# Performance work log

Hardware: AMD Instinct MI355X
Metric: run time of the kernel (lower is better)

Reference implementation:

```python
import jax, jax.numpy as jnp
import numpy as np

B, N = 128, 64
HID, MLP, DS, DV = 128, 128, 32, 32
DH = MLP - DS - DV  # 64
FILL = -10.0


def _embed_mask(x, W, b, fill):
    # Linear+ReLU on non-NaN rows; fill NaN rows with `fill` (matches embed_with_masking).
    nan = jnp.isnan(x).any(-1)
    e = jax.nn.relu(jnp.where(jnp.isnan(x), 0.0, x) @ W + b)
    return jnp.where(nan[..., None], jnp.asarray(fill, x.dtype), e)


def setup_inputs() -> dict:
    key = jax.random.key(0)
    ks = jax.random.split(key, 12)
    s = 0.05
    return {
        "hidden_states": jax.random.normal(ks[0], (B, N, HID), jnp.float32),
        "obs1": jax.random.normal(ks[1], (B, N, 2), jnp.float32),
        "obs2": jax.random.normal(ks[2], (B, N, 2), jnp.float32),
        "w_sp": jax.random.normal(ks[3], (2, DS), jnp.float32) * s,
        "b_sp": jnp.zeros((DS,), jnp.float32),
        "w_vel": jax.random.normal(ks[4], (2, DV), jnp.float32) * s,
        "b_vel": jnp.zeros((DV,), jnp.float32),
        "w_hid": jax.random.normal(ks[5], (HID, DH), jnp.float32) * s,
        "b_hid": jnp.zeros((DH,), jnp.float32),
        "wq": jax.random.normal(ks[6], (MLP, MLP), jnp.float32) * s,
        "wk": jax.random.normal(ks[7], (MLP, MLP), jnp.float32) * s,
        "wv": jax.random.normal(ks[8], (MLP, MLP), jnp.float32) * s,
        "in_proj_w": jax.random.normal(ks[9], (MLP, 3 * MLP), jnp.float32) * s,
        "in_proj_b": jnp.zeros((3 * MLP,), jnp.float32),
        "mha_out_w": jax.random.normal(ks[10], (MLP, MLP), jnp.float32) * s,
        "mha_out_b": jnp.zeros((MLP,), jnp.float32),
        "out_w": jax.random.normal(ks[11], (MLP, MLP), jnp.float32) * s,
        "out_b": jnp.zeros((MLP,), jnp.float32),
    }


def reference(hidden_states, obs1, obs2, w_sp, b_sp, w_vel, b_vel, w_hid, b_hid,
              wq, wk, wv, in_proj_w, in_proj_b, mha_out_w, mha_out_b, out_w, out_b):
    b, n = obs2.shape[0], obs2.shape[1]
    # relative positions: rel[b,i,j] = obs2[b,j] - obs2[b,i]
    rel = obs2[:, None, :, :] - obs2[:, :, None, :]              # [B,N,N,2]
    sp = _embed_mask(rel, w_sp, b_sp, FILL)                      # [B,N,N,DS]
    hid = _embed_mask(hidden_states, w_hid, b_hid, 0.0)          # [B,N,DH]
    hid_unf = jnp.broadcast_to(hid[:, None, :, :], (b, n, n, DH))
    vel = obs2 - obs1
    relvel = vel[:, None, :, :] - vel[:, :, None, :]             # [B,N,N,2]
    dv = _embed_mask(relvel * 4, w_vel, b_vel, FILL)             # [B,N,N,DV]
    emb = jnp.concatenate([sp, hid_unf, dv], axis=-1)            # [B,N,N,MLP]

    # MHA (1 head) in-proj weights split (stored as [in,out])
    w_iq, w_ik, w_iv = in_proj_w[:, :MLP], in_proj_w[:, MLP:2 * MLP], in_proj_w[:, 2 * MLP:]
    b_iq, b_ik, b_iv = in_proj_b[:MLP], in_proj_b[MLP:2 * MLP], in_proj_b[2 * MLP:]

    # Only the diagonal query position is kept by the final eye-mask gather,
    # and softmax rows are independent, so compute q only at j == i.
    idx = jnp.arange(n)
    emb_diag = emb[:, idx, idx]                                  # [B,N,MLP]
    q = (emb_diag @ wq) @ w_iq + b_iq                            # [B,N,MLP]
    k = (emb @ wk) @ w_ik + b_ik                                 # [B,N,N,MLP]
    v = (emb @ wv) @ w_iv + b_iv                                 # [B,N,N,MLP]

    scores = jnp.einsum('bid,bijd->bij', q, k) / jnp.sqrt(jnp.asarray(MLP, q.dtype))
    attn = jax.nn.softmax(scores, axis=-1)                       # [B,N,N]
    ctx = jnp.einsum('bij,bijd->bid', attn, v)                   # [B,N,MLP]
    mha_out = ctx @ mha_out_w + mha_out_b
    out = mha_out @ out_w + out_b                                # [B,N,out_dim]
    return out.reshape(b * n, -1)
```

## Files before the change

### kernel.cpp

```cpp
#include <hip/hip_runtime.h>

#define WS_WQC   0
#define WS_WKC   16384
#define WS_WVC   32768
#define WS_MOW   49152
#define WS_GQ    65536
#define WS_G0Q   73728
#define WS_FALL  73856
#define WS_FB    90240
#define WS_HID   90368
#define WS_NEED_HID_BYTES ((size_t)(90368 + 128*64*64) * 4)

__global__ __launch_bounds__(256) void precompute1(
    const float* __restrict__ wq, const float* __restrict__ wk,
    const float* __restrict__ wv, const float* __restrict__ in_proj_w,
    const float* __restrict__ mha_out_w, const float* __restrict__ out_w,
    const float* __restrict__ hs, const float* __restrict__ w_hid,
    const float* __restrict__ b_hid, float* __restrict__ ws)
{
    __shared__ __align__(16) float sbuf[4224];
    const int tid = threadIdx.x;

    if (blockIdx.x < 256) {
        const int mat  = blockIdx.x >> 6;
        const int rp   = blockIdx.x & 63;
        const int rsel = tid >> 7;
        const int col  = tid & 127;
        const int r    = 2 * rp + rsel;
        const float* A; const float* Bm; int ldb; float* C;
        if (mat == 0)      { A = wq;        Bm = in_proj_w;       ldb = 384; C = ws + WS_WQC; }
        else if (mat == 1) { A = wk;        Bm = in_proj_w + 128; ldb = 384; C = ws + WS_WKC; }
        else if (mat == 2) { A = wv;        Bm = in_proj_w + 256; ldb = 384; C = ws + WS_WVC; }
        else               { A = mha_out_w; Bm = out_w;           ldb = 128; C = ws + WS_MOW; }
        sbuf[tid] = A[r * 128 + col];
        __syncthreads();
        float acc = 0.f;
        #pragma unroll 8
        for (int d = 0; d < 128; ++d) acc = fmaf(sbuf[rsel * 128 + d], Bm[d * ldb + col], acc);
        C[r * 128 + col] = acc;
    } else {
        const int b2 = blockIdx.x - 256;
        const int b = b2 >> 1, half = b2 & 1;
        const float4* src = (const float4*)(hs + b * 8192 + half * 4096);
        for (int k = tid; k < 1024; k += 256) {
            const int row = k >> 5, c = k & 31;
            *(float4*)&sbuf[row * 132 + 4 * c] = src[k];
        }
        __syncthreads();
        const int ty = tid >> 4, tx = tid & 15;
        float a0c[4] = {0,0,0,0}, a1c[4] = {0,0,0,0};
        for (int d0 = 0; d0 < 128; d0 += 4) {
            const float4 a0 = *(const float4*)&sbuf[(2*ty+0)*132 + d0];
            const float4 a1 = *(const float4*)&sbuf[(2*ty+1)*132 + d0];
            const float* a0p = (const float*)&a0;
            const float* a1p = (const float*)&a1;
            #pragma unroll
            for (int dd = 0; dd < 4; ++dd) {
                const float4 w4 = *(const float4*)&w_hid[(d0+dd)*64 + 4*tx];
                a0c[0] = fmaf(a0p[dd], w4.x, a0c[0]); a0c[1] = fmaf(a0p[dd], w4.y, a0c[1]);
                a0c[2] = fmaf(a0p[dd], w4.z, a0c[2]); a0c[3] = fmaf(a0p[dd], w4.w, a0c[3]);
                a1c[0] = fmaf(a1p[dd], w4.x, a1c[0]); a1c[1] = fmaf(a1p[dd], w4.y, a1c[1]);
                a1c[2] = fmaf(a1p[dd], w4.z, a1c[2]); a1c[3] = fmaf(a1p[dd], w4.w, a1c[3]);
            }
        }
        const float4 bh = *(const float4*)&b_hid[4*tx];
        float* dst = ws + WS_HID + b * 4096 + (32*half + 2*ty) * 64 + 4*tx;
        *(float4*)dst        = make_float4(fmaxf(a0c[0]+bh.x,0.f), fmaxf(a0c[1]+bh.y,0.f),
                                           fmaxf(a0c[2]+bh.z,0.f), fmaxf(a0c[3]+bh.w,0.f));
        *(float4*)(dst + 64) = make_float4(fmaxf(a1c[0]+bh.x,0.f), fmaxf(a1c[1]+bh.y,0.f),
                                           fmaxf(a1c[2]+bh.z,0.f), fmaxf(a1c[3]+bh.w,0.f));
    }
}

__global__ __launch_bounds__(128) void precompute2(
    const float* __restrict__ b_sp, const float* __restrict__ b_vel,
    const float* __restrict__ in_proj_b, const float* __restrict__ mha_out_b,
    const float* __restrict__ out_w, const float* __restrict__ out_b,
    float* __restrict__ ws)
{
    const float* Wqc = ws + WS_WQC;
    const float* Wkc = ws + WS_WKC;
    const float* Wvc = ws + WS_WVC;
    const float* Mow = ws + WS_MOW;
    const int bid = blockIdx.x, tid = threadIdx.x;
    __shared__ float sa[128];

    if (bid < 64) {
        const int k = bid;
        sa[tid] = Wqc[(32 + k) * 128 + tid];
        __syncthreads();
        const int j = tid;
        const int pj = (j < 64) ? 32 + j : ((j < 96) ? j - 64 : j);
        const float* brow = Wkc + pj * 128;
        float acc = 0.f;
        #pragma unroll 8
        for (int d = 0; d < 128; ++d) acc = fmaf(sa[d], brow[d], acc);
        ws[WS_GQ + k * 128 + j] = acc;
    } else if (bid < 192) {
        const int k2 = bid - 64;
        const int srcRow = (k2 < 32) ? k2 : ((k2 < 64) ? 96 + (k2 - 32) : 32 + (k2 - 64));
        sa[tid] = Wvc[srcRow * 128 + tid];
        __syncthreads();
        float acc = 0.f;
        #pragma unroll 8
        for (int m = 0; m < 128; ++m) acc = fmaf(sa[m], Mow[m * 128 + tid], acc);
        ws[WS_FALL + k2 * 128 + tid] = acc;
    } else if (bid == 192) {
        float acc = out_b[tid];
        #pragma unroll 8
        for (int m = 0; m < 128; ++m) {
            acc = fmaf(in_proj_b[256 + m], Mow[m * 128 + tid], acc);
            acc = fmaf(mha_out_b[m], out_w[m * 128 + tid], acc);
        }
        ws[WS_FB + tid] = acc;
    } else {
        float qc = in_proj_b[tid];
        #pragma unroll 4
        for (int s = 0; s < 32; ++s) {
            qc = fmaf(fmaxf(b_sp[s], 0.f),  Wqc[s * 128 + tid], qc);
            qc = fmaf(fmaxf(b_vel[s], 0.f), Wqc[(96 + s) * 128 + tid], qc);
        }
        sa[tid] = qc;
        __syncthreads();
        const int j = tid;
        const int pj = (j < 64) ? 32 + j : ((j < 96) ? j - 64 : j);
        const float* brow = Wkc + pj * 128;
        float acc = 0.f;
        #pragma unroll 8
        for (int d = 0; d < 128; ++d) acc = fmaf(sa[d], brow[d], acc);
        ws[WS_G0Q + j] = acc;
    }
}

#define L_OBS  4224
#define L_WV   4480

template <bool HIDWS>
__global__ __launch_bounds__(256) void attn_main(
    const float* __restrict__ hs, const float* __restrict__ obs1,
    const float* __restrict__ obs2,
    const float* __restrict__ w_sp, const float* __restrict__ b_sp,
    const float* __restrict__ w_vel, const float* __restrict__ b_vel,
    const float* __restrict__ w_hid, const float* __restrict__ b_hid,
    const float* __restrict__ ws, float* __restrict__ out)
{
    const int tid = threadIdx.x;
    const int l   = tid & 63;
    const int w   = tid >> 6;
    const int b   = blockIdx.x >> 3;
    const int i0  = (blockIdx.x & 7) * 8;

    const float* GQ   = ws + WS_GQ;
    const float* g0q  = ws + WS_G0Q;
    const float* Fall = ws + WS_FALL;
    const float* fbv  = ws + WS_FB;

    __shared__ __align__(16) float smem[6016];
    float* const s_hid = smem;
    float* const s_obs = smem + L_OBS;
    float* const tt = smem + L_WV + w * 384;
    float* const qq = smem + L_WV + w * 384 + 128;
    float* const aa = smem + L_WV + w * 384 + 256;

    if (tid < 64) {
        const int g = b * 64 + tid;
        const float2 o2 = ((const float2*)obs2)[g];
        const float2 o1 = ((const float2*)obs1)[g];
        *(float4*)&s_obs[tid * 4] = make_float4(o2.x, o2.y, o2.x - o1.x, o2.y - o1.y);
    }
    if (HIDWS) {
        const float4* src = (const float4*)(ws + WS_HID + b * 4096);
        #pragma unroll
        for (int k = tid; k < 1024; k += 256) {
            const int row = k >> 4, c4 = (k & 15) * 4;
            const float4 v = src[k];
            *(float2*)&s_hid[row * 66 + c4]     = make_float2(v.x, v.y);
            *(float2*)&s_hid[row * 66 + c4 + 2] = make_float2(v.z, v.w);
        }
    } else {
        const int r = tid >> 2, qseg = (tid & 3) * 16;
        float acc[16];
        #pragma unroll
        for (int c = 0; c < 16; ++c) acc[c] = b_hid[qseg + c];
        for (int k = 0; k < 128; ++k) {
            const float a = hs[b * 8192 + r * 128 + k];
            #pragma unroll
            for (int c4 = 0; c4 < 4; ++c4) {
                const float4 w4 = *(const float4*)&w_hid[k * 64 + qseg + 4 * c4];
                acc[4*c4+0] = fmaf(a, w4.x, acc[4*c4+0]);
                acc[4*c4+1] = fmaf(a, w4.y, acc[4*c4+1]);
                acc[4*c4+2] = fmaf(a, w4.z, acc[4*c4+2]);
                acc[4*c4+3] = fmaf(a, w4.w, acc[4*c4+3]);
            }
        }
        #pragma unroll
        for (int c = 0; c < 16; c += 2)
            *(float2*)&s_hid[r * 66 + qseg + c] =
                make_float2(fmaxf(acc[c], 0.f), fmaxf(acc[c+1], 0.f));
    }
    __syncthreads();

    const int rg0 = i0 + 2 * w;

    {
        const float2 bias = *(const float2*)&g0q[2 * l];
        float a00 = bias.x, a01 = bias.y, a10 = bias.x, a11 = bias.y;
        const float* h0p = &s_hid[rg0 * 66];
        const float* h1p = &s_hid[(rg0 + 1) * 66];
        for (int k0 = 0; k0 < 64; k0 += 2) {
            const float2 h0 = *(const float2*)&h0p[k0];
            const float2 h1 = *(const float2*)&h1p[k0];
            const float2 g0v = *(const float2*)&GQ[k0 * 128 + 2 * l];
            const float2 g1v = *(const float2*)&GQ[(k0 + 1) * 128 + 2 * l];
            a00 = fmaf(h0.x, g0v.x, fmaf(h0.y, g1v.x, a00));
            a01 = fmaf(h0.x, g0v.y, fmaf(h0.y, g1v.y, a01));
            a10 = fmaf(h1.x, g0v.x, fmaf(h1.y, g1v.x, a10));
            a11 = fmaf(h1.x, g0v.y, fmaf(h1.y, g1v.y, a11));
        }
        if (l < 32) {
            *(float2*)&tt[2 * l]      = make_float2(a00, a01);
            *(float2*)&tt[64 + 2 * l] = make_float2(a10, a11);
        } else {
            *(float2*)&qq[2 * l - 64]  = make_float2(a00, a01);
            *(float2*)&qq[2 * l]       = make_float2(a10, a11);
        }
    }

    float sc0 = 0.f, sc1 = 0.f;
    {
        const float* hlp = &s_hid[l * 66];
        for (int c0 = 0; c0 < 64; c0 += 4) {
            const float4 t0 = *(const float4*)&tt[c0];
            const float4 t1 = *(const float4*)&tt[64 + c0];
            const float2 ha = *(const float2*)&hlp[c0];
            const float2 hb = *(const float2*)&hlp[c0 + 2];
            sc0 = fmaf(t0.x, ha.x, fmaf(t0.y, ha.y, fmaf(t0.z, hb.x, fmaf(t0.w, hb.y, sc0))));
            sc1 = fmaf(t1.x, ha.x, fmaf(t1.y, ha.y, fmaf(t1.z, hb.x, fmaf(t1.w, hb.y, sc1))));
        }
    }

    {
        const float4 oj  = *(const float4*)&s_obs[4 * l];
        const float4 oiA = *(const float4*)&s_obs[4 * rg0];
        const float4 oiB = *(const float4*)&s_obs[4 * (rg0 + 1)];
        const float rxA = oj.x - oiA.x, ryA = oj.y - oiA.y;
        const float dxA = (oj.z - oiA.z) * 4.f, dyA = (oj.w - oiA.w) * 4.f;
        const float rxB = oj.x - oiB.x, ryB = oj.y - oiB.y;
        const float dxB = (oj.z - oiB.z) * 4.f, dyB = (oj.w - oiB.w) * 4.f;
        float e0 = 0.f, e1 = 0.f;
        for (int s0 = 0; s0 < 32; s0 += 4) {
            const float4 qsA = *(const float4*)&qq[s0];
            const float4 qsB = *(const float4*)&qq[64 + s0];
            const float4 qdA = *(const float4*)&qq[32 + s0];
            const float4 qdB = *(const float4*)&qq[96 + s0];
            const float4 w0  = *(const float4*)&w_sp[s0];
            const float4 w1  = *(const float4*)&w_sp[32 + s0];
            const float4 bs  = *(const float4*)&b_sp[s0];
            const float4 wv0 = *(const float4*)&w_vel[s0];
            const float4 wv1 = *(const float4*)&w_vel[32 + s0];
            const float4 bv  = *(const float4*)&b_vel[s0];
            e0 = fmaf(qsA.x, fmaxf(fmaf(rxA, w0.x, fmaf(ryA, w1.x, bs.x)), 0.f), e0);
            e0 = fmaf(qsA.y, fmaxf(fmaf(rxA, w0.y, fmaf(ryA, w1.y, bs.y)), 0.f), e0);
            e0 = fmaf(qsA.z, fmaxf(fmaf(rxA, w0.z, fmaf(ryA, w1.z, bs.z)), 0.f), e0);
            e0 = fmaf(qsA.w, fmaxf(fmaf(rxA, w0.w, fmaf(ryA, w1.w, bs.w)), 0.f), e0);
            e0 = fmaf(qdA.x, fmaxf(fmaf(dxA, wv0.x, fmaf(dyA, wv1.x, bv.x)), 0.f), e0);
            e0 = fmaf(qdA.y, fmaxf(fmaf(dxA, wv0.y, fmaf(dyA, wv1.y, bv.y)), 0.f), e0);
            e0 = fmaf(qdA.z, fmaxf(fmaf(dxA, wv0.z, fmaf(dyA, wv1.z, bv.z)), 0.f), e0);
            e0 = fmaf(qdA.w, fmaxf(fmaf(dxA, wv0.w, fmaf(dyA, wv1.w, bv.w)), 0.f), e0);
            e1 = fmaf(qsB.x, fmaxf(fmaf(rxB, w0.x, fmaf(ryB, w1.x, bs.x)), 0.f), e1);
            e1 = fmaf(qsB.y, fmaxf(fmaf(rxB, w0.y, fmaf(ryB, w1.y, bs.y)), 0.f), e1);
            e1 = fmaf(qsB.z, fmaxf(fmaf(rxB, w0.z, fmaf(ryB, w1.z, bs.z)), 0.f), e1);
            e1 = fmaf(qsB.w, fmaxf(fmaf(rxB, w0.w, fmaf(ryB, w1.w, bs.w)), 0.f), e1);
            e1 = fmaf(qdB.x, fmaxf(fmaf(dxB, wv0.x, fmaf(dyB, wv1.x, bv.x)), 0.f), e1);
            e1 = fmaf(qdB.y, fmaxf(fmaf(dxB, wv0.y, fmaf(dyB, wv1.y, bv.y)), 0.f), e1);
            e1 = fmaf(qdB.z, fmaxf(fmaf(dxB, wv0.z, fmaf(dyB, wv1.z, bv.z)), 0.f), e1);
            e1 = fmaf(qdB.w, fmaxf(fmaf(dxB, wv0.w, fmaf(dyB, wv1.w, bv.w)), 0.f), e1);
        }
        const float scale = 0.08838834764831845f;
        float v0 = (sc0 + e0) * scale;
        float v1 = (sc1 + e1) * scale;
        float m0 = v0, m1 = v1;
        #pragma unroll
        for (int off = 32; off > 0; off >>= 1) {
            m0 = fmaxf(m0, __shfl_xor(m0, off, 64));
            m1 = fmaxf(m1, __shfl_xor(m1, off, 64));
        }
        const float ex0 = __expf(v0 - m0);
        const float ex1 = __expf(v1 - m1);
        float su0 = ex0, su1 = ex1;
        #pragma unroll
        for (int off = 32; off > 0; off >>= 1) {
            su0 += __shfl_xor(su0, off, 64);
            su1 += __shfl_xor(su1, off, 64);
        }
        *(float2*)&aa[2 * l] = make_float2(ex0 / su0, ex1 / su1);
    }

    {
        const int r = l >> 5, s = l & 31;
        const float w0 = w_sp[s],       w1 = w_sp[32 + s],  bsv = b_sp[s];
        const float u0 = w_vel[s],      u1 = w_vel[32 + s], bvv = b_vel[s];
        const float4 oi = *(const float4*)&s_obs[4 * (rg0 + r)];
        float ssp = 0.f, sdv = 0.f;
        for (int j0 = 0; j0 < 64; j0 += 2) {
            const float4 av  = *(const float4*)&aa[2 * j0];
            const float4 oj0 = *(const float4*)&s_obs[4 * j0];
            const float4 oj1 = *(const float4*)&s_obs[4 * j0 + 4];
            const float a0 = r ? av.y : av.x;
            const float a1 = r ? av.w : av.z;
            {
                const float rx = oj0.x - oi.x, ry = oj0.y - oi.y;
                const float dx = (oj0.z - oi.z) * 4.f, dy = (oj0.w - oi.w) * 4.f;
                ssp = fmaf(a0, fmaxf(fmaf(rx, w0, fmaf(ry, w1, bsv)), 0.f), ssp);
                sdv = fmaf(a0, fmaxf(fmaf(dx, u0, fmaf(dy, u1, bvv)), 0.f), sdv);
            }
            {
                const float rx = oj1.x - oi.x, ry = oj1.y - oi.y;
                const float dx = (oj1.z - oi.z) * 4.f, dy = (oj1.w - oi.w) * 4.f;
                ssp = fmaf(a1, fmaxf(fmaf(rx, w0, fmaf(ry, w1, bsv)), 0.f), ssp);
                sdv = fmaf(a1, fmaxf(fmaf(dx, u0, fmaf(dy, u1, bvv)), 0.f), sdv);
            }
        }
        tt[r * 64 + s]      = ssp;
        tt[r * 64 + 32 + s] = sdv;
    }

    {
        float ah0 = 0.f, ah1 = 0.f;
        for (int j0 = 0; j0 < 64; j0 += 2) {
            const float4 av = *(const float4*)&aa[2 * j0];
            const float h0 = s_hid[j0 * 66 + l];
            const float h1 = s_hid[(j0 + 1) * 66 + l];
            ah0 = fmaf(av.x, h0, fmaf(av.z, h1, ah0));
            ah1 = fmaf(av.y, h0, fmaf(av.w, h1, ah1));
        }
        qq[l]      = ah0;
        qq[64 + l] = ah1;
    }

    {
        const float2 fb2 = *(const float2*)&fbv[2 * l];
        float o00 = fb2.x, o01 = fb2.y, o10 = fb2.x, o11 = fb2.y;
        for (int k0 = 0; k0 < 64; k0 += 4) {
            const float4 A0 = *(const float4*)&tt[k0];
            const float4 A1 = *(const float4*)&tt[64 + k0];
            const float2 f0 = *(const float2*)&Fall[k0 * 128 + 2 * l];
            const float2 f1 = *(const float2*)&Fall[(k0 + 1) * 128 + 2 * l];
            const float2 f2 = *(const float2*)&Fall[(k0 + 2) * 128 + 2 * l];
            const float2 f3 = *(const float2*)&Fall[(k0 + 3) * 128 + 2 * l];
            o00 = fmaf(A0.x, f0.x, fmaf(A0.y, f1.x, fmaf(A0.z, f2.x, fmaf(A0.w, f3.x, o00))));
            o01 = fmaf(A0.x, f0.y, fmaf(A0.y, f1.y, fmaf(A0.z, f2.y, fmaf(A0.w, f3.y, o01))));
            o10 = fmaf(A1.x, f0.x, fmaf(A1.y, f1.x, fmaf(A1.z, f2.x, fmaf(A1.w, f3.x, o10))));
            o11 = fmaf(A1.x, f0.y, fmaf(A1.y, f1.y, fmaf(A1.z, f2.y, fmaf(A1.w, f3.y, o11))));
        }
        for (int k0 = 0; k0 < 64; k0 += 4) {
            const float4 A0 = *(const float4*)&qq[k0];
            const float4 A1 = *(const float4*)&qq[64 + k0];
            const float2 f0 = *(const float2*)&Fall[(64 + k0) * 128 + 2 * l];
            const float2 f1 = *(const float2*)&Fall[(65 + k0) * 128 + 2 * l];
            const float2 f2 = *(const float2*)&Fall[(66 + k0) * 128 + 2 * l];
            const float2 f3 = *(const float2*)&Fall[(67 + k0) * 128 + 2 * l];
            o00 = fmaf(A0.x, f0.x, fmaf(A0.y, f1.x, fmaf(A0.z, f2.x, fmaf(A0.w, f3.x, o00))));
            o01 = fmaf(A0.x, f0.y, fmaf(A0.y, f1.y, fmaf(A0.z, f2.y, fmaf(A0.w, f3.y, o01))));
            o10 = fmaf(A1.x, f0.x, fmaf(A1.y, f1.x, fmaf(A1.z, f2.x, fmaf(A1.w, f3.x, o10))));
            o11 = fmaf(A1.x, f0.y, fmaf(A1.y, f1.y, fmaf(A1.z, f2.y, fmaf(A1.w, f3.y, o11))));
        }
        const int gr = (b * 64 + rg0) * 128 + 2 * l;
        *(float2*)&out[gr]       = make_float2(o00, o01);
        *(float2*)&out[gr + 128] = make_float2(o10, o11);
    }
}

extern "C" void kernel_launch(void* const* d_in, const int* in_sizes, int n_in,
                              void* d_out, int out_size, void* d_ws, size_t ws_size,
                              hipStream_t stream) {
    const float* hs        = (const float*)d_in[0];
    const float* obs1      = (const float*)d_in[1];
    const float* obs2      = (const float*)d_in[2];
    const float* w_sp      = (const float*)d_in[3];
    const float* b_sp      = (const float*)d_in[4];
    const float* w_vel     = (const float*)d_in[5];
    const float* b_vel     = (const float*)d_in[6];
    const float* w_hid     = (const float*)d_in[7];
    const float* b_hid     = (const float*)d_in[8];
    const float* wq        = (const float*)d_in[9];
    const float* wk        = (const float*)d_in[10];
    const float* wv        = (const float*)d_in[11];
    const float* in_proj_w = (const float*)d_in[12];
    const float* in_proj_b = (const float*)d_in[13];
    const float* mha_out_w = (const float*)d_in[14];
    const float* mha_out_b = (const float*)d_in[15];
    const float* out_w     = (const float*)d_in[16];
    const float* out_b     = (const float*)d_in[17];
    float* ws  = (float*)d_ws;
    float* out = (float*)d_out;

    const bool hidws = (ws_size >= WS_NEED_HID_BYTES);

    precompute1<<<hidws ? 512 : 256, 256, 0, stream>>>(
        wq, wk, wv, in_proj_w, mha_out_w, out_w, hs, w_hid, b_hid, ws);
    precompute2<<<194, 128, 0, stream>>>(
        b_sp, b_vel, in_proj_b, mha_out_b, out_w, out_b, ws);
    if (hidws) {
        attn_main<true><<<1024, 256, 0, stream>>>(hs, obs1, obs2, w_sp, b_sp, w_vel, b_vel,
                                                  w_hid, b_hid, ws, out);
    } else {
        attn_main<false><<<1024, 256, 0, stream>>>(hs, obs1, obs2, w_sp, b_sp, w_vel, b_vel,
                                                   w_hid, b_hid, ws, out);
    }
}
```

Measured before the change: 140.4 us.

## Process four query rows per wave and use packed FP32 FMA

Result: faster. 128.9 us (-8.2%).

```diff
diff --git a/kernel.cpp b/kernel.cpp
--- a/kernel.cpp
+++ b/kernel.cpp
@@ -1,4 +1,15 @@
 #include <hip/hip_runtime.h>
+#include <string.h>
+
+typedef float v2f __attribute__((ext_vector_type(2)));
+#define PKFMA(a,b,c) __builtin_elementwise_fma((a),(b),(c))
+#define PKMAX(a,b)   __builtin_elementwise_max((a),(b))
+static __device__ __forceinline__ v2f vsplat(float s) { return (v2f){s, s}; }
+static __device__ __forceinline__ v2f shfl_xor_v2(v2f x, int m) {
+    double d = __builtin_bit_cast(double, x);
+    d = __shfl_xor(d, m, 64);
+    return __builtin_bit_cast(v2f, d);
+}
 
 #define WS_WQC   0
 #define WS_WKC   16384
@@ -147,20 +158,21 @@
     const int tid = threadIdx.x;
     const int l   = tid & 63;
     const int w   = tid >> 6;
-    const int b   = blockIdx.x >> 3;
-    const int i0  = (blockIdx.x & 7) * 8;
+    const int b   = blockIdx.x >> 2;
+    const int i0  = (blockIdx.x & 3) * 16;
+    const int rg0 = i0 + 4 * w;
 
     const float* GQ   = ws + WS_GQ;
     const float* g0q  = ws + WS_G0Q;
     const float* Fall = ws + WS_FALL;
     const float* fbv  = ws + WS_FB;
 
-    __shared__ __align__(16) float smem[6016];
+    __shared__ __align__(16) float smem[7552];
     float* const s_hid = smem;
     float* const s_obs = smem + L_OBS;
-    float* const tt = smem + L_WV + w * 384;
-    float* const qq = smem + L_WV + w * 384 + 128;
-    float* const aa = smem + L_WV + w * 384 + 256;
+    float* const tt = smem + L_WV + w * 768;
+    float* const qq = smem + L_WV + w * 768 + 256;
+    float* const aa = smem + L_WV + w * 768 + 512;
 
     if (tid < 64) {
         const int g = b * 64 + tid;
@@ -174,8 +186,8 @@
         for (int k = tid; k < 1024; k += 256) {
             const int row = k >> 4, c4 = (k & 15) * 4;
             const float4 v = src[k];
-            *(float2*)&s_hid[row * 66 + c4]     = make_float2(v.x, v.y);
-            *(float2*)&s_hid[row * 66 + c4 + 2] = make_float2(v.z, v.w);
+            *(v2f*)&s_hid[row * 66 + c4]     = (v2f){v.x, v.y};
+            *(v2f*)&s_hid[row * 66 + c4 + 2] = (v2f){v.z, v.w};
         }
     } else {
         const int r = tid >> 2, qseg = (tid & 3) * 16;
@@ -195,179 +207,180 @@
         }
         #pragma unroll
         for (int c = 0; c < 16; c += 2)
-            *(float2*)&s_hid[r * 66 + qseg + c] =
-                make_float2(fmaxf(acc[c], 0.f), fmaxf(acc[c+1], 0.f));
+            *(v2f*)&s_hid[r * 66 + qseg + c] =
+                (v2f){fmaxf(acc[c], 0.f), fmaxf(acc[c+1], 0.f)};
     }
     __syncthreads();
 
-    const int rg0 = i0 + 2 * w;
-
-    {
-        const float2 bias = *(const float2*)&g0q[2 * l];
-        float a00 = bias.x, a01 = bias.y, a10 = bias.x, a11 = bias.y;
-        const float* h0p = &s_hid[rg0 * 66];
-        const float* h1p = &s_hid[(rg0 + 1) * 66];
+    {
+        const v2f bias = *(const v2f*)&g0q[2 * l];
+        v2f acc0 = bias, acc1 = bias, acc2 = bias, acc3 = bias;
         for (int k0 = 0; k0 < 64; k0 += 2) {
-            const float2 h0 = *(const float2*)&h0p[k0];
-            const float2 h1 = *(const float2*)&h1p[k0];
-            const float2 g0v = *(const float2*)&GQ[k0 * 128 + 2 * l];
-            const float2 g1v = *(const float2*)&GQ[(k0 + 1) * 128 + 2 * l];
-            a00 = fmaf(h0.x, g0v.x, fmaf(h0.y, g1v.x, a00));
-            a01 = fmaf(h0.x, g0v.y, fmaf(h0.y, g1v.y, a01));
-            a10 = fmaf(h1.x, g0v.x, fmaf(h1.y, g1v.x, a10));
-            a11 = fmaf(h1.x, g0v.y, fmaf(h1.y, g1v.y, a11));
+            const v2f g0 = *(const v2f*)&GQ[k0 * 128 + 2 * l];
+            const v2f g1 = *(const v2f*)&GQ[(k0 + 1) * 128 + 2 * l];
+            const v2f h0 = *(const v2f*)&s_hid[(rg0 + 0) * 66 + k0];
+            const v2f h1 = *(const v2f*)&s_hid[(rg0 + 1) * 66 + k0];
+            const v2f h2 = *(const v2f*)&s_hid[(rg0 + 2) * 66 + k0];
+            const v2f h3 = *(const v2f*)&s_hid[(rg0 + 3) * 66 + k0];
+            acc0 = PKFMA(vsplat(h0.x), g0, PKFMA(vsplat(h0.y), g1, acc0));
+            acc1 = PKFMA(vsplat(h1.x), g0, PKFMA(vsplat(h1.y), g1, acc1));
+            acc2 = PKFMA(vsplat(h2.x), g0, PKFMA(vsplat(h2.y), g1, acc2));
+            acc3 = PKFMA(vsplat(h3.x), g0, PKFMA(vsplat(h3.y), g1, acc3));
         }
         if (l < 32) {
-            *(float2*)&tt[2 * l]      = make_float2(a00, a01);
-            *(float2*)&tt[64 + 2 * l] = make_float2(a10, a11);
+            const int c = 2 * l;
+            *(v2f*)&tt[0 * 64 + c] = acc0;  *(v2f*)&tt[1 * 64 + c] = acc1;
+            *(v2f*)&tt[2 * 64 + c] = acc2;  *(v2f*)&tt[3 * 64 + c] = acc3;
         } else {
-            *(float2*)&qq[2 * l - 64]  = make_float2(a00, a01);
-            *(float2*)&qq[2 * l]       = make_float2(a10, a11);
-        }
-    }
-
-    float sc0 = 0.f, sc1 = 0.f;
-    {
-        const float* hlp = &s_hid[l * 66];
-        for (int c0 = 0; c0 < 64; c0 += 4) {
-            const float4 t0 = *(const float4*)&tt[c0];
-            const float4 t1 = *(const float4*)&tt[64 + c0];
-            const float2 ha = *(const float2*)&hlp[c0];
-            const float2 hb = *(const float2*)&hlp[c0 + 2];
-            sc0 = fmaf(t0.x, ha.x, fmaf(t0.y, ha.y, fmaf(t0.z, hb.x, fmaf(t0.w, hb.y, sc0))));
-            sc1 = fmaf(t1.x, ha.x, fmaf(t1.y, ha.y, fmaf(t1.z, hb.x, fmaf(t1.w, hb.y, sc1))));
-        }
-    }
-
-    {
-        const float4 oj  = *(const float4*)&s_obs[4 * l];
-        const float4 oiA = *(const float4*)&s_obs[4 * rg0];
-        const float4 oiB = *(const float4*)&s_obs[4 * (rg0 + 1)];
-        const float rxA = oj.x - oiA.x, ryA = oj.y - oiA.y;
-        const float dxA = (oj.z - oiA.z) * 4.f, dyA = (oj.w - oiA.w) * 4.f;
-        const float rxB = oj.x - oiB.x, ryB = oj.y - oiB.y;
-        const float dxB = (oj.z - oiB.z) * 4.f, dyB = (oj.w - oiB.w) * 4.f;
-        float e0 = 0.f, e1 = 0.f;
-        for (int s0 = 0; s0 < 32; s0 += 4) {
-            const float4 qsA = *(const float4*)&qq[s0];
-            const float4 qsB = *(const float4*)&qq[64 + s0];
-            const float4 qdA = *(const float4*)&qq[32 + s0];
-            const float4 qdB = *(const float4*)&qq[96 + s0];
-            const float4 w0  = *(const float4*)&w_sp[s0];
-            const float4 w1  = *(const float4*)&w_sp[32 + s0];
-            const float4 bs  = *(const float4*)&b_sp[s0];
-            const float4 wv0 = *(const float4*)&w_vel[s0];
-            const float4 wv1 = *(const float4*)&w_vel[32 + s0];
-            const float4 bv  = *(const float4*)&b_vel[s0];
-            e0 = fmaf(qsA.x, fmaxf(fmaf(rxA, w0.x, fmaf(ryA, w1.x, bs.x)), 0.f), e0);
-            e0 = fmaf(qsA.y, fmaxf(fmaf(rxA, w0.y, fmaf(ryA, w1.y, bs.y)), 0.f), e0);
-            e0 = fmaf(qsA.z, fmaxf(fmaf(rxA, w0.z, fmaf(ryA, w1.z, bs.z)), 0.f), e0);
-            e0 = fmaf(qsA.w, fmaxf(fmaf(rxA, w0.w, fmaf(ryA, w1.w, bs.w)), 0.f), e0);
-            e0 = fmaf(qdA.x, fmaxf(fmaf(dxA, wv0.x, fmaf(dyA, wv1.x, bv.x)), 0.f), e0);
-            e0 = fmaf(qdA.y, fmaxf(fmaf(dxA, wv0.y, fmaf(dyA, wv1.y, bv.y)), 0.f), e0);
-            e0 = fmaf(qdA.z, fmaxf(fmaf(dxA, wv0.z, fmaf(dyA, wv1.z, bv.z)), 0.f), e0);
-            e0 = fmaf(qdA.w, fmaxf(fmaf(dxA, wv0.w, fmaf(dyA, wv1.w, bv.w)), 0.f), e0);
-            e1 = fmaf(qsB.x, fmaxf(fmaf(rxB, w0.x, fmaf(ryB, w1.x, bs.x)), 0.f), e1);
-            e1 = fmaf(qsB.y, fmaxf(fmaf(rxB, w0.y, fmaf(ryB, w1.y, bs.y)), 0.f), e1);
-            e1 = fmaf(qsB.z, fmaxf(fmaf(rxB, w0.z, fmaf(ryB, w1.z, bs.z)), 0.f), e1);
-            e1 = fmaf(qsB.w, fmaxf(fmaf(rxB, w0.w, fmaf(ryB, w1.w, bs.w)), 0.f), e1);
-            e1 = fmaf(qdB.x, fmaxf(fmaf(dxB, wv0.x, fmaf(dyB, wv1.x, bv.x)), 0.f), e1);
-            e1 = fmaf(qdB.y, fmaxf(fmaf(dxB, wv0.y, fmaf(dyB, wv1.y, bv.y)), 0.f), e1);
-            e1 = fmaf(qdB.z, fmaxf(fmaf(dxB, wv0.z, fmaf(dyB, wv1.z, bv.z)), 0.f), e1);
-            e1 = fmaf(qdB.w, fmaxf(fmaf(dxB, wv0.w, fmaf(dyB, wv1.w, bv.w)), 0.f), e1);
+            const int c = 2 * l - 64;
+            *(v2f*)&qq[0 * 64 + c] = acc0;  *(v2f*)&qq[1 * 64 + c] = acc1;
+            *(v2f*)&qq[2 * 64 + c] = acc2;  *(v2f*)&qq[3 * 64 + c] = acc3;
+        }
+    }
+
+    float sc[4];
+    {
+        v2f s0 = (v2f){0.f,0.f}, s1 = s0, s2 = s0, s3 = s0;
+        const float* hl = &s_hid[l * 66];
+        for (int c0 = 0; c0 < 64; c0 += 2) {
+            const v2f h2 = *(const v2f*)&hl[c0];
+            s0 = PKFMA(*(const v2f*)&tt[0 * 64 + c0], h2, s0);
+            s1 = PKFMA(*(const v2f*)&tt[1 * 64 + c0], h2, s1);
+            s2 = PKFMA(*(const v2f*)&tt[2 * 64 + c0], h2, s2);
+            s3 = PKFMA(*(const v2f*)&tt[3 * 64 + c0], h2, s3);
+        }
+        sc[0] = s0.x + s0.y; sc[1] = s1.x + s1.y;
+        sc[2] = s2.x + s2.y; sc[3] = s3.x + s3.y;
+    }
+
+    {
+        const float4 oj = *(const float4*)&s_obs[4 * l];
+        float rx[4], ry[4], dx[4], dy[4];
+        #pragma unroll
+        for (int r = 0; r < 4; ++r) {
+            const float4 oi = *(const float4*)&s_obs[4 * (rg0 + r)];
+            rx[r] = oj.x - oi.x;  ry[r] = oj.y - oi.y;
+            dx[r] = (oj.z - oi.z) * 4.f;  dy[r] = (oj.w - oi.w) * 4.f;
+        }
+        v2f acc[4] = {{0,0},{0,0},{0,0},{0,0}};
+        for (int s0 = 0; s0 < 32; s0 += 2) {
+            const v2f w0p = *(const v2f*)&w_sp[s0];
+            const v2f w1p = *(const v2f*)&w_sp[32 + s0];
+            const v2f bsp = *(const v2f*)&b_sp[s0];
+            const v2f u0p = *(const v2f*)&w_vel[s0];
+            const v2f u1p = *(const v2f*)&w_vel[32 + s0];
+            const v2f bvp = *(const v2f*)&b_vel[s0];
+            #pragma unroll
+            for (int r = 0; r < 4; ++r) {
+                const v2f qs2 = *(const v2f*)&qq[r * 64 + s0];
+                const v2f qd2 = *(const v2f*)&qq[r * 64 + 32 + s0];
+                const v2f esp = PKMAX(PKFMA(vsplat(rx[r]), w0p,
+                                     PKFMA(vsplat(ry[r]), w1p, bsp)), vsplat(0.f));
+                acc[r] = PKFMA(qs2, esp, acc[r]);
+                const v2f edv = PKMAX(PKFMA(vsplat(dx[r]), u0p,
+                                     PKFMA(vsplat(dy[r]), u1p, bvp)), vsplat(0.f));
+                acc[r] = PKFMA(qd2, edv, acc[r]);
+            }
         }
         const float scale = 0.08838834764831845f;
-        float v0 = (sc0 + e0) * scale;
-        float v1 = (sc1 + e1) * scale;
-        float m0 = v0, m1 = v1;
+        v2f p01 = (v2f){(sc[0] + acc[0].x + acc[0].y) * scale,
+                        (sc[1] + acc[1].x + acc[1].y) * scale};
+        v2f p23 = (v2f){(sc[2] + acc[2].x + acc[2].y) * scale,
+                        (sc[3] + acc[3].x + acc[3].y) * scale};
+        v2f m01 = p01, m23 = p23;
         #pragma unroll
         for (int off = 32; off > 0; off >>= 1) {
-            m0 = fmaxf(m0, __shfl_xor(m0, off, 64));
-            m1 = fmaxf(m1, __shfl_xor(m1, off, 64));
-        }
-        const float ex0 = __expf(v0 - m0);
-        const float ex1 = __expf(v1 - m1);
-        float su0 = ex0, su1 = ex1;
+            m01 = PKMAX(m01, shfl_xor_v2(m01, off));
+            m23 = PKMAX(m23, shfl_xor_v2(m23, off));
+        }
+        v2f e01 = (v2f){__expf(p01.x - m01.x), __expf(p01.y - m01.y)};
+        v2f e23 = (v2f){__expf(p23.x - m23.x), __expf(p23.y - m23.y)};
+        v2f u01 = e01, u23 = e23;
         #pragma unroll
         for (int off = 32; off > 0; off >>= 1) {
-            su0 += __shfl_xor(su0, off, 64);
-            su1 += __shfl_xor(su1, off, 64);
-        }
-        *(float2*)&aa[2 * l] = make_float2(ex0 / su0, ex1 / su1);
-    }
-
-    {
-        const int r = l >> 5, s = l & 31;
-        const float w0 = w_sp[s],       w1 = w_sp[32 + s],  bsv = b_sp[s];
-        const float u0 = w_vel[s],      u1 = w_vel[32 + s], bvv = b_vel[s];
+            u01 = u01 + shfl_xor_v2(u01, off);
+            u23 = u23 + shfl_xor_v2(u23, off);
+        }
+        *(float4*)&aa[4 * l] = make_float4(e01.x / u01.x, e01.y / u01.y,
+                                           e23.x / u23.x, e23.y / u23.y);
+    }
+
+    {
+        const int r = l >> 4, s = l & 15;
+        const v2f w0p = (v2f){w_sp[s],        w_sp[s + 16]};
+        const v2f w1p = (v2f){w_sp[32 + s],   w_sp[48 + s]};
+        const v2f bsp = (v2f){b_sp[s],        b_sp[s + 16]};
+        const v2f u0p = (v2f){w_vel[s],       w_vel[s + 16]};
+        const v2f u1p = (v2f){w_vel[32 + s],  w_vel[48 + s]};
+        const v2f bvp = (v2f){b_vel[s],       b_vel[s + 16]};
         const float4 oi = *(const float4*)&s_obs[4 * (rg0 + r)];
-        float ssp = 0.f, sdv = 0.f;
-        for (int j0 = 0; j0 < 64; j0 += 2) {
-            const float4 av  = *(const float4*)&aa[2 * j0];
-            const float4 oj0 = *(const float4*)&s_obs[4 * j0];
-            const float4 oj1 = *(const float4*)&s_obs[4 * j0 + 4];
-            const float a0 = r ? av.y : av.x;
-            const float a1 = r ? av.w : av.z;
-            {
-                const float rx = oj0.x - oi.x, ry = oj0.y - oi.y;
-                const float dx = (oj0.z - oi.z) * 4.f, dy = (oj0.w - oi.w) * 4.f;
-                ssp = fmaf(a0, fmaxf(fmaf(rx, w0, fmaf(ry, w1, bsv)), 0.f), ssp);
-                sdv = fmaf(a0, fmaxf(fmaf(dx, u0, fmaf(dy, u1, bvv)), 0.f), sdv);
-            }
-            {
-                const float rx = oj1.x - oi.x, ry = oj1.y - oi.y;
-                const float dx = (oj1.z - oi.z) * 4.f, dy = (oj1.w - oi.w) * 4.f;
-                ssp = fmaf(a1, fmaxf(fmaf(rx, w0, fmaf(ry, w1, bsv)), 0.f), ssp);
-                sdv = fmaf(a1, fmaxf(fmaf(dx, u0, fmaf(dy, u1, bvv)), 0.f), sdv);
-            }
-        }
-        tt[r * 64 + s]      = ssp;
-        tt[r * 64 + 32 + s] = sdv;
-    }
-
-    {
-        float ah0 = 0.f, ah1 = 0.f;
-        for (int j0 = 0; j0 < 64; j0 += 2) {
-            const float4 av = *(const float4*)&aa[2 * j0];
-            const float h0 = s_hid[j0 * 66 + l];
-            const float h1 = s_hid[(j0 + 1) * 66 + l];
-            ah0 = fmaf(av.x, h0, fmaf(av.z, h1, ah0));
-            ah1 = fmaf(av.y, h0, fmaf(av.w, h1, ah1));
-        }
-        qq[l]      = ah0;
-        qq[64 + l] = ah1;
-    }
-
-    {
-        const float2 fb2 = *(const float2*)&fbv[2 * l];
-        float o00 = fb2.x, o01 = fb2.y, o10 = fb2.x, o11 = fb2.y;
-        for (int k0 = 0; k0 < 64; k0 += 4) {
-            const float4 A0 = *(const float4*)&tt[k0];
-            const float4 A1 = *(const float4*)&tt[64 + k0];
-            const float2 f0 = *(const float2*)&Fall[k0 * 128 + 2 * l];
-            const float2 f1 = *(const float2*)&Fall[(k0 + 1) * 128 + 2 * l];
-            const float2 f2 = *(const float2*)&Fall[(k0 + 2) * 128 + 2 * l];
-            const float2 f3 = *(const float2*)&Fall[(k0 + 3) * 128 + 2 * l];
-            o00 = fmaf(A0.x, f0.x, fmaf(A0.y, f1.x, fmaf(A0.z, f2.x, fmaf(A0.w, f3.x, o00))));
-            o01 = fmaf(A0.x, f0.y, fmaf(A0.y, f1.y, fmaf(A0.z, f2.y, fmaf(A0.w, f3.y, o01))));
-            o10 = fmaf(A1.x, f0.x, fmaf(A1.y, f1.x, fmaf(A1.z, f2.x, fmaf(A1.w, f3.x, o10))));
-            o11 = fmaf(A1.x, f0.y, fmaf(A1.y, f1.y, fmaf(A1.z, f2.y, fmaf(A1.w, f3.y, o11))));
-        }
-        for (int k0 = 0; k0 < 64; k0 += 4) {
-            const float4 A0 = *(const float4*)&qq[k0];
-            const float4 A1 = *(const float4*)&qq[64 + k0];
-            const float2 f0 = *(const float2*)&Fall[(64 + k0) * 128 + 2 * l];
-            const float2 f1 = *(const float2*)&Fall[(65 + k0) * 128 + 2 * l];
-            const float2 f2 = *(const float2*)&Fall[(66 + k0) * 128 + 2 * l];
-            const float2 f3 = *(const float2*)&Fall[(67 + k0) * 128 + 2 * l];
-            o00 = fmaf(A0.x, f0.x, fmaf(A0.y, f1.x, fmaf(A0.z, f2.x, fmaf(A0.w, f3.x, o00))));
-            o01 = fmaf(A0.x, f0.y, fmaf(A0.y, f1.y, fmaf(A0.z, f2.y, fmaf(A0.w, f3.y, o01))));
-            o10 = fmaf(A1.x, f0.x, fmaf(A1.y, f1.x, fmaf(A1.z, f2.x, fmaf(A1.w, f3.x, o10))));
-            o11 = fmaf(A1.x, f0.y, fmaf(A1.y, f1.y, fmaf(A1.z, f2.y, fmaf(A1.w, f3.y, o11))));
+        v2f asp = (v2f){0.f, 0.f}, adv = asp;
+        for (int j = 0; j < 64; ++j) {
+            const float a = aa[4 * j + r];
+            const float4 o4 = *(const float4*)&s_obs[4 * j];
+            const float rxx = o4.x - oi.x, ryy = o4.y - oi.y;
+            const float dxx = (o4.z - oi.z) * 4.f, dyy = (o4.w - oi.w) * 4.f;
+            const v2f esp = PKMAX(PKFMA(vsplat(rxx), w0p,
+                                 PKFMA(vsplat(ryy), w1p, bsp)), vsplat(0.f));
+            asp = PKFMA(vsplat(a), esp, asp);
+            const v2f edv = PKMAX(PKFMA(vsplat(dxx), u0p,
+                                 PKFMA(vsplat(dyy), u1p, bvp)), vsplat(0.f));
+            adv = PKFMA(vsplat(a), edv, adv);
+        }
+        tt[r * 64 + s]           = asp.x;
+        tt[r * 64 + s + 16]      = asp.y;
+        tt[r * 64 + 32 + s]      = adv.x;
+        tt[r * 64 + 48 + s]      = adv.y;
+    }
+
+    {
+        float ah0 = 0.f, ah1 = 0.f, ah2 = 0.f, ah3 = 0.f;
+        for (int j = 0; j < 64; j += 2) {
+            const float4 a0 = *(const float4*)&aa[4 * j];
+            const float4 a1 = *(const float4*)&aa[4 * j + 4];
+            const float h0 = s_hid[j * 66 + l];
+            const float h1 = s_hid[(j + 1) * 66 + l];
+            ah0 = fmaf(a0.x, h0, fmaf(a1.x, h1, ah0));
+            ah1 = fmaf(a0.y, h0, fmaf(a1.y, h1, ah1));
+            ah2 = fmaf(a0.z, h0, fmaf(a1.z, h1, ah2));
+            ah3 = fmaf(a0.w, h0, fmaf(a1.w, h1, ah3));
+        }
+        qq[0 * 64 + l] = ah0;  qq[1 * 64 + l] = ah1;
+        qq[2 * 64 + l] = ah2;  qq[3 * 64 + l] = ah3;
+    }
+
+    {
+        const v2f fb2 = *(const v2f*)&fbv[2 * l];
+        v2f o0 = fb2, o1 = fb2, o2 = fb2, o3 = fb2;
+        for (int k = 0; k < 64; k += 2) {
+            const v2f f0 = *(const v2f*)&Fall[k * 128 + 2 * l];
+            const v2f f1 = *(const v2f*)&Fall[(k + 1) * 128 + 2 * l];
+            const v2f A0 = *(const v2f*)&tt[0 * 64 + k];
+            const v2f A1 = *(const v2f*)&tt[1 * 64 + k];
+            const v2f A2 = *(const v2f*)&tt[2 * 64 + k];
+            const v2f A3 = *(const v2f*)&tt[3 * 64 + k];
+            o0 = PKFMA(vsplat(A0.x), f0, PKFMA(vsplat(A0.y), f1, o0));
+            o1 = PKFMA(vsplat(A1.x), f0, PKFMA(vsplat(A1.y), f1, o1));
+            o2 = PKFMA(vsplat(A2.x), f0, PKFMA(vsplat(A2.y), f1, o2));
+            o3 = PKFMA(vsplat(A3.x), f0, PKFMA(vsplat(A3.y), f1, o3));
+        }
+        for (int k = 0; k < 64; k += 2) {
+            const v2f f0 = *(const v2f*)&Fall[(64 + k) * 128 + 2 * l];
+            const v2f f1 = *(const v2f*)&Fall[(65 + k) * 128 + 2 * l];
+            const v2f A0 = *(const v2f*)&qq[0 * 64 + k];
+            const v2f A1 = *(const v2f*)&qq[1 * 64 + k];
+            const v2f A2 = *(const v2f*)&qq[2 * 64 + k];
+            const v2f A3 = *(const v2f*)&qq[3 * 64 + k];
+            o0 = PKFMA(vsplat(A0.x), f0, PKFMA(vsplat(A0.y), f1, o0));
+            o1 = PKFMA(vsplat(A1.x), f0, PKFMA(vsplat(A1.y), f1, o1));
+            o2 = PKFMA(vsplat(A2.x), f0, PKFMA(vsplat(A2.y), f1, o2));
+            o3 = PKFMA(vsplat(A3.x), f0, PKFMA(vsplat(A3.y), f1, o3));
         }
         const int gr = (b * 64 + rg0) * 128 + 2 * l;
-        *(float2*)&out[gr]       = make_float2(o00, o01);
-        *(float2*)&out[gr + 128] = make_float2(o10, o11);
+        *(v2f*)&out[gr]           = o0;
+        *(v2f*)&out[gr + 128]     = o1;
+        *(v2f*)&out[gr + 256]     = o2;
+        *(v2f*)&out[gr + 384]     = o3;
     }
 }
 
@@ -402,10 +415,10 @@
     precompute2<<<194, 128, 0, stream>>>(
         b_sp, b_vel, in_proj_b, mha_out_b, out_w, out_b, ws);
     if (hidws) {
-        attn_main<true><<<1024, 256, 0, stream>>>(hs, obs1, obs2, w_sp, b_sp, w_vel, b_vel,
+        attn_main<true><<<512, 256, 0, stream>>>(hs, obs1, obs2, w_sp, b_sp, w_vel, b_vel,
+                                                 w_hid, b_hid, ws, out);
+    } else {
+        attn_main<false><<<512, 256, 0, stream>>>(hs, obs1, obs2, w_sp, b_sp, w_vel, b_vel,
                                                   w_hid, b_hid, ws, out);
-    } else {
-        attn_main<false><<<1024, 256, 0, stream>>>(hs, obs1, obs2, w_sp, b_sp, w_vel, b_vel,
-                                                   w_hid, b_hid, ws, out);
     }
 }
```
